# Performance work log

Hardware: AMD Instinct MI355X
Metric: run time of the kernel (lower is better)

## Reference

```python
import jax, jax.numpy as jnp
import numpy as np

D_MODEL = 1024
NUM_HEADS = 16
D_K = D_MODEL // NUM_HEADS


def setup_inputs() -> dict:
    key = jax.random.key(0)
    ks = jax.random.split(key, 7)
    B, S = 2, 2048
    query = jax.random.normal(ks[0], (B, S, D_MODEL), dtype=jnp.float32)
    key_t = jax.random.normal(ks[1], (B, S, D_MODEL), dtype=jnp.float32)
    value = jax.random.normal(ks[2], (B, S, D_MODEL), dtype=jnp.float32)
    attention_mask = jnp.ones((B, S), dtype=jnp.int32)
    # xavier_uniform for square d_model x d_model: limit = sqrt(6/(fan_in+fan_out))
    limit = np.sqrt(6.0 / (D_MODEL + D_MODEL)).astype(np.float32)
    def xav(k):
        return jax.random.uniform(k, (D_MODEL, D_MODEL), dtype=jnp.float32, minval=-limit, maxval=limit)
    return {
        "query": query, "key": key_t, "value": value,
        "attention_mask": attention_mask,
        "w_q": xav(ks[3]), "w_k": xav(ks[4]), "w_v": xav(ks[5]), "w_o": xav(ks[6]),
    }


def reference(query, key, value, attention_mask, w_q, w_k, w_v, w_o):
    B, S, _ = query.shape
    # torch Linear: x @ W.T  (weights stored [out, in])
    def proj(x, w):
        y = jnp.einsum('bsd,ed->bse', x, w)
        return y.reshape(B, S, NUM_HEADS, D_K).transpose(0, 2, 1, 3)  # [B,H,S,Dk]
    q = proj(query, w_q)
    k = proj(key, w_k)
    v = proj(value, w_v)
    scores = jnp.einsum('bhqd,bhkd->bhqk', q, k) / jnp.sqrt(jnp.float32(D_K))
    # mask [B,S] -> [B,1,1,S]; masked_fill where mask == 0
    mask = (attention_mask[:, None, None, :] == 0)
    scores = jnp.where(mask, jnp.float32(-1e9), scores)
    attn = jax.nn.softmax(scores, axis=-1)
    # dropout p=0.0 (eval) -> identity
    context = jnp.einsum('bhqk,bhkd->bhqd', attn, v)
    context = context.transpose(0, 2, 1, 3).reshape(B, S, D_MODEL)
    return jnp.einsum('bsd,ed->bse', context, w_o)
```

## Files before the change

### kernel.cpp

```cpp
#include <hip/hip_runtime.h>
#include <hip/hip_bf16.h>


typedef short short8  __attribute__((ext_vector_type(8)));
typedef short short4v __attribute__((ext_vector_type(4)));
typedef float f32x4   __attribute__((ext_vector_type(4)));

#define D_MODEL 1024
#define SEQ     2048
#define NHEAD   16
#define DKD     64
#define HSTR    (SEQ * DKD)
#define QSCALE  0.1803368801111204f
#define EXP2F(x) exp2f(x)

#define MFMA16(a, b, c) __builtin_amdgcn_mfma_f32_16x16x32_bf16((a), (b), (c), 0, 0, 0)

__device__ __forceinline__ ushort f2bf(float f) {
    __hip_bfloat16 h = __float2bfloat16(f);
    return __builtin_bit_cast(ushort, h);
}

__device__ __forceinline__ short8 frag128(const ushort* base, int row, int c0) {
    int cb = (c0 * 2) ^ ((row & 7) << 4);
    return *(const short8*)((const char*)base + row * 128 + cb);
}
__device__ __forceinline__ short8 frag256(const ushort* base, int row, int c0) {
    int cb = (c0 * 2) ^ ((row & 7) << 4);
    return *(const short8*)((const char*)base + row * 256 + cb);
}

__global__ __launch_bounds__(256) void cvt_w(
    const float* __restrict__ s0, const float* __restrict__ s1, const float* __restrict__ s2,
    ushort* __restrict__ dst)
{
    const int z = blockIdx.y;
    const float* s = (z == 0) ? s0 : ((z == 1) ? s1 : s2);
    ushort* d = dst + (size_t)z * 1048576;
    const int i = (blockIdx.x * 256 + threadIdx.x) * 8;
    f32x4 a = *(const f32x4*)(s + i);
    f32x4 b = *(const f32x4*)(s + i + 4);
    short8 o;
    #pragma unroll
    for (int u = 0; u < 4; ++u) { o[u] = (short)f2bf(a[u]); o[4 + u] = (short)f2bf(b[u]); }
    *(short8*)(d + i) = o;
}

template<int LAYOUT, int A_BF16>
__global__ __launch_bounds__(256, 3) void gemm_nt(
    const void* __restrict__ A0, const void* __restrict__ A1, const void* __restrict__ A2,
    const ushort* __restrict__ W0, const ushort* __restrict__ W1, const ushort* __restrict__ W2,
    void* __restrict__ O0, void* __restrict__ O1, void* __restrict__ O2)
{
    const int z = blockIdx.z;
    const void*   A = (z == 0) ? A0 : ((z == 1) ? A1 : A2);
    const ushort* W = (z == 0) ? W0 : ((z == 1) ? W1 : W2);
    void* O         = (z == 0) ? O0 : ((z == 1) ? O1 : O2);

    const int bm = blockIdx.x * 128;
    const int bn = blockIdx.y * 128;
    const int tid = threadIdx.x;
    const int w = tid >> 6, l = tid & 63;
    const int wr = w >> 1, wc = w & 1;

    __shared__ ushort sm[16384];

    f32x4 acc[4][4] = {};
    short8 areg[4], wreg[4];
    const int srow = tid >> 3;
    const int sc8  = (tid & 7) << 3;
    const int scb  = (sc8 * 2);

    #define GLOADT(t_) {                                                                    \
        _Pragma("unroll")                                                                   \
        for (int i = 0; i < 4; ++i) {                                                       \
            int row = i * 32 + srow;                                                        \
            if (A_BF16) {                                                                   \
                areg[i] = *(const short8*)((const ushort*)A + (size_t)(bm + row) * 1024 + (t_) * 64 + sc8); \
            } else {                                                                        \
                const float* ap = (const float*)A + (size_t)(bm + row) * 1024 + (t_) * 64 + sc8; \
                f32x4 x0 = *(const f32x4*)ap, x1 = *(const f32x4*)(ap + 4);                 \
                _Pragma("unroll")                                                           \
                for (int u = 0; u < 4; ++u) { areg[i][u] = (short)f2bf(x0[u]); areg[i][4 + u] = (short)f2bf(x1[u]); } \
            }                                                                               \
            wreg[i] = *(const short8*)(W + (size_t)(bn + row) * 1024 + (t_) * 64 + sc8);    \
        } }

    #define GWRITET() {                                                                     \
        _Pragma("unroll")                                                                   \
        for (int i = 0; i < 4; ++i) {                                                       \
            int row = i * 32 + srow;                                                        \
            int cb  = scb ^ ((row & 7) << 4);                                               \
            *(short8*)((char*)sm + row * 128 + cb) = areg[i];                               \
            *(short8*)((char*)(sm + 8192) + row * 128 + cb) = wreg[i];                      \
        } }

    GLOADT(0);
    #pragma unroll 1
    for (int t = 0; t < 16; ++t) {
        GWRITET();
        __syncthreads();
        if (t < 15) GLOADT(t + 1);

        #pragma unroll
        for (int kk = 0; kk < 2; ++kk) {
            const int c0 = kk * 32 + ((l >> 4) << 3);
            short8 af[4], bf[4];
            #pragma unroll
            for (int mi = 0; mi < 4; ++mi)
                af[mi] = frag128(sm, wr * 64 + mi * 16 + (l & 15), c0);
            #pragma unroll
            for (int ni = 0; ni < 4; ++ni)
                bf[ni] = frag128(sm + 8192, wc * 64 + ni * 16 + (l & 15), c0);
            #pragma unroll
            for (int mi = 0; mi < 4; ++mi)
                #pragma unroll
                for (int ni = 0; ni < 4; ++ni)
                    acc[mi][ni] = MFMA16(af[mi], bf[ni], acc[mi][ni]);
        }
        __syncthreads();
    }
    #undef GLOADT
    #undef GWRITET

    if (LAYOUT == 0 && z == 2) {
        #pragma unroll
        for (int mi = 0; mi < 4; ++mi) {
            #pragma unroll
            for (int ni = 0; ni < 4; ++ni) {
                int n_l = wc * 64 + ni * 16 + (l & 15);
                int m0  = wr * 64 + mi * 16 + ((l >> 4) << 2);
                short4v v4;
                #pragma unroll
                for (int j = 0; j < 4; ++j) v4[j] = (short)f2bf(acc[mi][ni][j]);
                *(short4v*)((char*)sm + n_l * 256 + ((m0 * 2) ^ ((n_l & 7) << 4))) = v4;
            }
        }
        __syncthreads();
        const int row = tid >> 1, half = tid & 1;
        const int n_g = bn + row;
        const int bb  = bm >> 11;
        ushort* Op = (ushort*)O + (size_t)(bb * NHEAD + (n_g >> 6)) * HSTR
                     + (size_t)(n_g & 63) * SEQ + (bm & 2047) + half * 64;
        #pragma unroll
        for (int u = 0; u < 8; ++u) {
            short8 c = *(const short8*)((char*)sm + row * 256
                        + (((half * 64 + u * 8) * 2) ^ ((row & 7) << 4)));
            *(short8*)(Op + u * 8) = c;
        }
        return;
    }

    const float sc = (LAYOUT == 0 && z == 0) ? QSCALE : 1.0f;
    #pragma unroll
    for (int mi = 0; mi < 4; ++mi) {
        #pragma unroll
        for (int ni = 0; ni < 4; ++ni) {
            #pragma unroll
            for (int j = 0; j < 4; ++j) {
                int m = bm + wr * 64 + mi * 16 + ((l >> 4) << 2) + j;
                int n = bn + wc * 64 + ni * 16 + (l & 15);
                if (LAYOUT == 0) {
                    int b = m >> 11, s = m & 2047, h = n >> 6, dk = n & 63;
                    ((ushort*)O)[(size_t)(b * NHEAD + h) * HSTR + s * DKD + dk] = f2bf(acc[mi][ni][j] * sc);
                } else {
                    ((float*)O)[(size_t)m * 1024 + n] = acc[mi][ni][j];
                }
            }
        }
    }
}

__global__ __launch_bounds__(256, 2) void attn_fwd(
    const ushort* __restrict__ Q, const ushort* __restrict__ K, const ushort* __restrict__ Vt,
    const int* __restrict__ mask, ushort* __restrict__ ctx)
{
    const int tid = threadIdx.x;
    const int w = tid >> 6, l = tid & 63;
    const int hi = l >> 4, lo = l & 15;
    const int id  = blockIdx.x;
    const int nid = (id & 7) * 64 + (id >> 3);
    const int bh  = nid >> 4;
    const int q0  = (nid & 15) * 128;
    const int b   = bh >> 4, h = bh & 15;

    __shared__ ushort sm[2][16384];
    __shared__ int mflag;

    if (tid == 0) mflag = 1;
    __syncthreads();
    {
        const int4* mp = ((const int4*)(mask + b * SEQ)) + tid;
        int4 m0 = mp[0], m1 = mp[256];
        if (!(m0.x && m0.y && m0.z && m0.w && m1.x && m1.y && m1.z && m1.w)) mflag = 0;
    }

    const ushort* Qh = Q  + (size_t)bh * HSTR;
    const ushort* Kh = K  + (size_t)bh * HSTR;
    const ushort* Vh = Vt + (size_t)bh * HSTR;

    short8 qf[2][2];
    #pragma unroll
    for (int g = 0; g < 2; ++g)
        #pragma unroll
        for (int kk = 0; kk < 2; ++kk)
            qf[g][kk] = *(const short8*)(Qh + (size_t)(q0 + w * 32 + g * 16 + lo) * DKD
                                         + kk * 32 + hi * 8);

    f32x4 acc[2][4] = {};
    float m_run[2] = {-INFINITY, -INFINITY}, l_run[2] = {0.0f, 0.0f};

    const int kr = tid >> 3;
    const int kc = (tid & 7) << 3;
    const int vr = tid >> 4;
    const int vkpb = (tid & 15) << 4;

    short8  kreg[4];
    short4v vreg0[4], vreg1[4];

    #define LOADT(kt_) {                                                                   \
        _Pragma("unroll")                                                                  \
        for (int i = 0; i < 4; ++i)                                                        \
            kreg[i] = *(const short8*)(Kh + (size_t)((kt_) * 128 + i * 32 + kr) * DKD + kc); \
        _Pragma("unroll")                                                                  \
        for (int i = 0; i < 4; ++i) {                                                      \
            const ushort* vp = Vh + (size_t)(i * 16 + vr) * SEQ + (kt_) * 128 + ((tid >> 2) & 3) * 32 + (tid & 3) * 4; \
            vreg0[i] = *(const short4v*)(vp);                                              \
            vreg1[i] = *(const short4v*)(vp + 16); } }

    #define WRITET(buf_) {                                                                 \
        _Pragma("unroll")                                                                  \
        for (int i = 0; i < 4; ++i) {                                                      \
            int r = i * 32 + kr;                                                           \
            *(short8*)((char*)sm[buf_] + r * 128 + ((kc * 2) ^ ((r & 7) << 4))) = kreg[i]; } \
        _Pragma("unroll")                                                                  \
        for (int i = 0; i < 4; ++i) {                                                      \
            int r = i * 16 + vr;                                                           \
            char* p = (char*)(sm[buf_] + 8192) + r * 256 + (vkpb ^ ((r & 7) << 4));        \
            *(short4v*)(p)     = vreg0[i];                                                 \
            *(short4v*)(p + 8) = vreg1[i]; } }

    LOADT(0); WRITET(0);
    __syncthreads();
    const bool allones = (mflag != 0);
    const f32x4 zf = {};

    #define SMG(g_) {                                                                      \
        if (!allones) {                                                                    \
            const int* mrow = mask + b * SEQ + kt * 128 + hi * 4;                          \
            _Pragma("unroll")                                                              \
            for (int ni = 0; ni < 8; ++ni) {                                               \
                int4 mv = *(const int4*)(mrow + ni * 16);                                  \
                s4[g_][ni][0] = mv.x ? s4[g_][ni][0] : -1e9f;                              \
                s4[g_][ni][1] = mv.y ? s4[g_][ni][1] : -1e9f;                              \
                s4[g_][ni][2] = mv.z ? s4[g_][ni][2] : -1e9f;                              \
                s4[g_][ni][3] = mv.w ? s4[g_][ni][3] : -1e9f;                              \
            }                                                                              \
        }                                                                                  \
        float t = fmaxf(fmaxf(s4[g_][0][0], s4[g_][0][1]), fmaxf(s4[g_][0][2], s4[g_][0][3])); \
        _Pragma("unroll")                                                                  \
        for (int ni = 1; ni < 8; ++ni) {                                                   \
            float tn = fmaxf(fmaxf(s4[g_][ni][0], s4[g_][ni][1]),                          \
                             fmaxf(s4[g_][ni][2], s4[g_][ni][3]));                         \
            t = fmaxf(t, tn);                                                              \
        }                                                                                  \
        t = fmaxf(t, __shfl_xor(t, 16));                                                   \
        t = fmaxf(t, __shfl_xor(t, 32));                                                   \
        if (!__all(t <= m_run[g_] + 8.0f)) {                                               \
            float mnew = fmaxf(m_run[g_], t);                                              \
            float c = EXP2F(m_run[g_] - mnew);                                             \
            m_run[g_] = mnew;                                                              \
            l_run[g_] *= c;                                                                \
            float cj[4];                                                                   \
            _Pragma("unroll")                                                              \
            for (int j = 0; j < 4; ++j) cj[j] = __shfl(c, (l & 48) | (hi * 4 + j));        \
            _Pragma("unroll")                                                              \
            for (int ni = 0; ni < 4; ++ni)                                                 \
                _Pragma("unroll")                                                          \
                for (int j = 0; j < 4; ++j) acc[g_][ni][j] *= cj[j];                       \
        }                                                                                  \
        float rs = 0.0f;                                                                   \
        _Pragma("unroll")                                                                  \
        for (int ni = 0; ni < 8; ++ni) {                                                   \
            _Pragma("unroll")                                                              \
            for (int j = 0; j < 4; ++j) s4[g_][ni][j] = EXP2F(s4[g_][ni][j] - m_run[g_]);  \
            rs += (s4[g_][ni][0] + s4[g_][ni][1]) + (s4[g_][ni][2] + s4[g_][ni][3]);       \
        }                                                                                  \
        rs += __shfl_xor(rs, 16);                                                          \
        rs += __shfl_xor(rs, 32);                                                          \
        l_run[g_] += rs;                                                                   \
        _Pragma("unroll")                                                                  \
        for (int kk = 0; kk < 4; ++kk)                                                     \
            _Pragma("unroll")                                                              \
            for (int j = 0; j < 4; ++j) {                                                  \
                pa[g_][kk][j]     = (short)f2bf(s4[g_][2 * kk][j]);                        \
                pa[g_][kk][4 + j] = (short)f2bf(s4[g_][2 * kk + 1][j]);                    \
            } }

    #pragma unroll 1
    for (int kt = 0; kt < 16; ++kt) {
        const int cur = kt & 1;
        const ushort* kb = sm[cur];
        const ushort* vb = sm[cur] + 8192;

        if (kt < 15) LOADT(kt + 1);

        f32x4 s4[2][8];
        __builtin_amdgcn_s_setprio(1);
        #pragma unroll
        for (int ni = 0; ni < 8; ++ni) {
            short8 kf = frag128(kb, ni * 16 + lo, hi * 8);
            s4[0][ni] = MFMA16(kf, qf[0][0], zf);
            s4[1][ni] = MFMA16(kf, qf[1][0], zf);
        }
        #pragma unroll
        for (int ni = 0; ni < 8; ++ni) {
            short8 kf = frag128(kb, ni * 16 + lo, 32 + hi * 8);
            s4[0][ni] = MFMA16(kf, qf[0][1], s4[0][ni]);
            s4[1][ni] = MFMA16(kf, qf[1][1], s4[1][ni]);
        }
        __builtin_amdgcn_s_setprio(0);

        short8 pa[2][4];
        SMG(0)
        SMG(1)

        if (kt < 15) WRITET(cur ^ 1);

        __builtin_amdgcn_s_setprio(1);
        #pragma unroll
        for (int kk = 0; kk < 4; ++kk) {
            const int c0 = kk * 32 + hi * 8;
            #pragma unroll
            for (int ni = 0; ni < 4; ++ni) {
                short8 vf = frag256(vb, ni * 16 + lo, c0);
                acc[0][ni] = MFMA16(pa[0][kk], vf, acc[0][ni]);
                acc[1][ni] = MFMA16(pa[1][kk], vf, acc[1][ni]);
            }
        }
        __builtin_amdgcn_s_setprio(0);

        __syncthreads();
    }
    #undef SMG
    #undef LOADT
    #undef WRITET

    #pragma unroll
    for (int g = 0; g < 2; ++g) {
        float inv = 1.0f / l_run[g];
        float invj[4];
        #pragma unroll
        for (int j = 0; j < 4; ++j)
            invj[j] = __shfl(inv, (l & 48) | (hi * 4 + j));
        #pragma unroll
        for (int ni = 0; ni < 4; ++ni)
            #pragma unroll
            for (int j = 0; j < 4; ++j) {
                int qg = q0 + w * 32 + g * 16 + hi * 4 + j;
                ctx[(size_t)(b * SEQ + qg) * D_MODEL + h * DKD + ni * 16 + lo] =
                    f2bf(acc[g][ni][j] * invj[j]);
            }
    }
}

__global__ void ws_sentinel(float* __restrict__ out, int n, float code) {
    int i = blockIdx.x * blockDim.x + threadIdx.x;
    if (i < n) out[i] = (i == 0) ? code : 0.0f;
}

extern "C" void kernel_launch(void* const* d_in, const int* in_sizes, int n_in,
                              void* d_out, int out_size, void* d_ws, size_t ws_size,
                              hipStream_t stream) {
    const float* q    = (const float*)d_in[0];
    const float* k    = (const float*)d_in[1];
    const float* v    = (const float*)d_in[2];
    const int*   mask = (const int*)d_in[3];
    const float* wq   = (const float*)d_in[4];
    const float* wk   = (const float*)d_in[5];
    const float* wv   = (const float*)d_in[6];
    const float* wo   = (const float*)d_in[7];
    float* out = (float*)d_out;

    if (ws_size < (size_t)33554432) {
        float code = 100.0f + (float)(ws_size >> 20);
        ws_sentinel<<<(out_size + 255) / 256, 256, 0, stream>>>(out, out_size, code);
        return;
    }

    ushort* ws = (ushort*)d_ws;
    ushort* Qb = ws;
    ushort* Kb = ws + 4194304;
    ushort* Vb = ws + 8388608;
    ushort* Cb = ws + 12582912;

    dim3 blk(256, 1, 1);
    cvt_w<<<dim3(512, 3), blk, 0, stream>>>(wq, wk, wv, Cb);
    gemm_nt<0, 0><<<dim3(32, 8, 3), blk, 0, stream>>>(
        q, k, v, Cb, Cb + 1048576, Cb + 2097152, Qb, Kb, Vb);
    attn_fwd<<<dim3(512, 1, 1), blk, 0, stream>>>(Qb, Kb, Vb, mask, Cb);
    cvt_w<<<dim3(512, 1), blk, 0, stream>>>(wo, wo, wo, Qb);
    gemm_nt<1, 1><<<dim3(32, 8, 1), blk, 0, stream>>>(
        Cb, Cb, Cb, Qb, Qb, Qb, out, out, out);
}
```

Baseline: 136.4 us.

## Split attention KV tile across two wave groups with LDS merge of partial softmax

Doubles the attention block to 512 threads: two groups of four waves each process half of every 128-key tile for the same query rows, keeping separate running max/sum and accumulators. The groups are merged at the end through shared memory using log-sum-exp rescaling. This halves per-wave register and instruction work per tile to raise occupancy and latency hiding, at the cost of a final LDS reduction and more waves contending for the same tiles. It also switches exp2 to the hardware builtin.

```diff
diff --git a/kernel.cpp b/kernel.cpp
--- a/kernel.cpp
+++ b/kernel.cpp
@@ -12,7 +12,7 @@
 #define DKD     64
 #define HSTR    (SEQ * DKD)
 #define QSCALE  0.1803368801111204f
-#define EXP2F(x) exp2f(x)
+#define EXP2F(x) __builtin_amdgcn_exp2f(x)
 
 #define MFMA16(a, b, c) __builtin_amdgcn_mfma_f32_16x16x32_bf16((a), (b), (c), 0, 0, 0)
 
@@ -171,13 +171,14 @@
     }
 }
 
-__global__ __launch_bounds__(256, 2) void attn_fwd(
+__global__ __launch_bounds__(512, 4) void attn_fwd(
     const ushort* __restrict__ Q, const ushort* __restrict__ K, const ushort* __restrict__ Vt,
     const int* __restrict__ mask, ushort* __restrict__ ctx)
 {
     const int tid = threadIdx.x;
     const int w = tid >> 6, l = tid & 63;
     const int hi = l >> 4, lo = l & 15;
+    const int g = w >> 2, wq = w & 3;
     const int id  = blockIdx.x;
     const int nid = (id & 7) * 64 + (id >> 3);
     const int bh  = nid >> 4;
@@ -190,9 +191,8 @@
     if (tid == 0) mflag = 1;
     __syncthreads();
     {
-        const int4* mp = ((const int4*)(mask + b * SEQ)) + tid;
-        int4 m0 = mp[0], m1 = mp[256];
-        if (!(m0.x && m0.y && m0.z && m0.w && m1.x && m1.y && m1.z && m1.w)) mflag = 0;
+        int4 m0 = ((const int4*)(mask + b * SEQ))[tid];
+        if (!(m0.x && m0.y && m0.z && m0.w)) mflag = 0;
     }
 
     const ushort* Qh = Q  + (size_t)bh * HSTR;
@@ -201,13 +201,13 @@
 
     short8 qf[2][2];
     #pragma unroll
-    for (int g = 0; g < 2; ++g)
+    for (int gq = 0; gq < 2; ++gq)
         #pragma unroll
         for (int kk = 0; kk < 2; ++kk)
-            qf[g][kk] = *(const short8*)(Qh + (size_t)(q0 + w * 32 + g * 16 + lo) * DKD
-                                         + kk * 32 + hi * 8);
-
-    f32x4 acc[2][4] = {};
+            qf[gq][kk] = *(const short8*)(Qh + (size_t)(q0 + wq * 32 + gq * 16 + lo) * DKD
+                                          + kk * 32 + hi * 8);
+
+    f32x4 acc_o[2][4] = {};
     float m_run[2] = {-INFINITY, -INFINITY}, l_run[2] = {0.0f, 0.0f};
 
     const int kr = tid >> 3;
@@ -215,27 +215,27 @@
     const int vr = tid >> 4;
     const int vkpb = (tid & 15) << 4;
 
-    short8  kreg[4];
-    short4v vreg0[4], vreg1[4];
+    short8  kreg[2];
+    short4v vreg0[2], vreg1[2];
 
     #define LOADT(kt_) {                                                                   \
         _Pragma("unroll")                                                                  \
-        for (int i = 0; i < 4; ++i)                                                        \
-            kreg[i] = *(const short8*)(Kh + (size_t)((kt_) * 128 + i * 32 + kr) * DKD + kc); \
-        _Pragma("unroll")                                                                  \
-        for (int i = 0; i < 4; ++i) {                                                      \
-            const ushort* vp = Vh + (size_t)(i * 16 + vr) * SEQ + (kt_) * 128 + ((tid >> 2) & 3) * 32 + (tid & 3) * 4; \
+        for (int i = 0; i < 2; ++i)                                                        \
+            kreg[i] = *(const short8*)(Kh + (size_t)((kt_) * 128 + i * 64 + kr) * DKD + kc); \
+        _Pragma("unroll")                                                                  \
+        for (int i = 0; i < 2; ++i) {                                                      \
+            const ushort* vp = Vh + (size_t)(i * 32 + vr) * SEQ + (kt_) * 128 + ((tid >> 2) & 3) * 32 + (tid & 3) * 4; \
             vreg0[i] = *(const short4v*)(vp);                                              \
             vreg1[i] = *(const short4v*)(vp + 16); } }
 
     #define WRITET(buf_) {                                                                 \
         _Pragma("unroll")                                                                  \
-        for (int i = 0; i < 4; ++i) {                                                      \
-            int r = i * 32 + kr;                                                           \
+        for (int i = 0; i < 2; ++i) {                                                      \
+            int r = i * 64 + kr;                                                           \
             *(short8*)((char*)sm[buf_] + r * 128 + ((kc * 2) ^ ((r & 7) << 4))) = kreg[i]; } \
         _Pragma("unroll")                                                                  \
-        for (int i = 0; i < 4; ++i) {                                                      \
-            int r = i * 16 + vr;                                                           \
+        for (int i = 0; i < 2; ++i) {                                                      \
+            int r = i * 32 + vr;                                                           \
             char* p = (char*)(sm[buf_] + 8192) + r * 256 + (vkpb ^ ((r & 7) << 4));        \
             *(short4v*)(p)     = vreg0[i];                                                 \
             *(short4v*)(p + 8) = vreg1[i]; } }
@@ -245,56 +245,44 @@
     const bool allones = (mflag != 0);
     const f32x4 zf = {};
 
-    #define SMG(g_) {                                                                      \
-        if (!allones) {                                                                    \
-            const int* mrow = mask + b * SEQ + kt * 128 + hi * 4;                          \
-            _Pragma("unroll")                                                              \
-            for (int ni = 0; ni < 8; ++ni) {                                               \
-                int4 mv = *(const int4*)(mrow + ni * 16);                                  \
-                s4[g_][ni][0] = mv.x ? s4[g_][ni][0] : -1e9f;                              \
-                s4[g_][ni][1] = mv.y ? s4[g_][ni][1] : -1e9f;                              \
-                s4[g_][ni][2] = mv.z ? s4[g_][ni][2] : -1e9f;                              \
-                s4[g_][ni][3] = mv.w ? s4[g_][ni][3] : -1e9f;                              \
-            }                                                                              \
-        }                                                                                  \
-        float t = fmaxf(fmaxf(s4[g_][0][0], s4[g_][0][1]), fmaxf(s4[g_][0][2], s4[g_][0][3])); \
-        _Pragma("unroll")                                                                  \
-        for (int ni = 1; ni < 8; ++ni) {                                                   \
-            float tn = fmaxf(fmaxf(s4[g_][ni][0], s4[g_][ni][1]),                          \
-                             fmaxf(s4[g_][ni][2], s4[g_][ni][3]));                         \
-            t = fmaxf(t, tn);                                                              \
-        }                                                                                  \
+    #define SMG(gq_) {                                                                     \
+        float t = fmaxf(fmaxf(s4[gq_][0][0], s4[gq_][0][1]),                               \
+                        fmaxf(s4[gq_][0][2], s4[gq_][0][3]));                              \
+        _Pragma("unroll")                                                                  \
+        for (int ni = 1; ni < 4; ++ni)                                                     \
+            t = fmaxf(t, fmaxf(fmaxf(s4[gq_][ni][0], s4[gq_][ni][1]),                      \
+                               fmaxf(s4[gq_][ni][2], s4[gq_][ni][3])));                    \
         t = fmaxf(t, __shfl_xor(t, 16));                                                   \
         t = fmaxf(t, __shfl_xor(t, 32));                                                   \
-        if (!__all(t <= m_run[g_] + 8.0f)) {                                               \
-            float mnew = fmaxf(m_run[g_], t);                                              \
-            float c = EXP2F(m_run[g_] - mnew);                                             \
-            m_run[g_] = mnew;                                                              \
-            l_run[g_] *= c;                                                                \
+        if (!__all(t <= m_run[gq_] + 8.0f)) {                                              \
+            float mnew = fmaxf(m_run[gq_], t);                                             \
+            float c = EXP2F(m_run[gq_] - mnew);                                            \
+            m_run[gq_] = mnew;                                                             \
+            l_run[gq_] *= c;                                                               \
             float cj[4];                                                                   \
             _Pragma("unroll")                                                              \
             for (int j = 0; j < 4; ++j) cj[j] = __shfl(c, (l & 48) | (hi * 4 + j));        \
             _Pragma("unroll")                                                              \
             for (int ni = 0; ni < 4; ++ni)                                                 \
                 _Pragma("unroll")                                                          \
-                for (int j = 0; j < 4; ++j) acc[g_][ni][j] *= cj[j];                       \
+                for (int j = 0; j < 4; ++j) acc_o[gq_][ni][j] *= cj[j];                    \
         }                                                                                  \
         float rs = 0.0f;                                                                   \
         _Pragma("unroll")                                                                  \
-        for (int ni = 0; ni < 8; ++ni) {                                                   \
+        for (int ni = 0; ni < 4; ++ni) {                                                   \
             _Pragma("unroll")                                                              \
-            for (int j = 0; j < 4; ++j) s4[g_][ni][j] = EXP2F(s4[g_][ni][j] - m_run[g_]);  \
-            rs += (s4[g_][ni][0] + s4[g_][ni][1]) + (s4[g_][ni][2] + s4[g_][ni][3]);       \
+            for (int j = 0; j < 4; ++j) s4[gq_][ni][j] = EXP2F(s4[gq_][ni][j] - m_run[gq_]); \
+            rs += (s4[gq_][ni][0] + s4[gq_][ni][1]) + (s4[gq_][ni][2] + s4[gq_][ni][3]);   \
         }                                                                                  \
         rs += __shfl_xor(rs, 16);                                                          \
         rs += __shfl_xor(rs, 32);                                                          \
-        l_run[g_] += rs;                                                                   \
-        _Pragma("unroll")                                                                  \
-        for (int kk = 0; kk < 4; ++kk)                                                     \
+        l_run[gq_] += rs;                                                                  \
+        _Pragma("unroll")                                                                  \
+        for (int kk = 0; kk < 2; ++kk)                                                     \
             _Pragma("unroll")                                                              \
             for (int j = 0; j < 4; ++j) {                                                  \
-                pa[g_][kk][j]     = (short)f2bf(s4[g_][2 * kk][j]);                        \
-                pa[g_][kk][4 + j] = (short)f2bf(s4[g_][2 * kk + 1][j]);                    \
+                pa[gq_][kk][j]     = (short)f2bf(s4[gq_][2 * kk][j]);                      \
+                pa[gq_][kk][4 + j] = (short)f2bf(s4[gq_][2 * kk + 1][j]);                  \
             } }
 
     #pragma unroll 1
@@ -305,23 +293,38 @@
 
         if (kt < 15) LOADT(kt + 1);
 
-        f32x4 s4[2][8];
+        f32x4 s4[2][4];
         __builtin_amdgcn_s_setprio(1);
         #pragma unroll
-        for (int ni = 0; ni < 8; ++ni) {
-            short8 kf = frag128(kb, ni * 16 + lo, hi * 8);
+        for (int ni = 0; ni < 4; ++ni) {
+            short8 kf = frag128(kb, g * 64 + ni * 16 + lo, hi * 8);
             s4[0][ni] = MFMA16(kf, qf[0][0], zf);
             s4[1][ni] = MFMA16(kf, qf[1][0], zf);
         }
         #pragma unroll
-        for (int ni = 0; ni < 8; ++ni) {
-            short8 kf = frag128(kb, ni * 16 + lo, 32 + hi * 8);
+        for (int ni = 0; ni < 4; ++ni) {
+            short8 kf = frag128(kb, g * 64 + ni * 16 + lo, 32 + hi * 8);
             s4[0][ni] = MFMA16(kf, qf[0][1], s4[0][ni]);
             s4[1][ni] = MFMA16(kf, qf[1][1], s4[1][ni]);
         }
         __builtin_amdgcn_s_setprio(0);
 
-        short8 pa[2][4];
+        if (!allones) {
+            const int* mrow = mask + b * SEQ + kt * 128 + g * 64 + hi * 4;
+            #pragma unroll
+            for (int ni = 0; ni < 4; ++ni) {
+                int4 mv = *(const int4*)(mrow + ni * 16);
+                #pragma unroll
+                for (int gq = 0; gq < 2; ++gq) {
+                    s4[gq][ni][0] = mv.x ? s4[gq][ni][0] : -1e9f;
+                    s4[gq][ni][1] = mv.y ? s4[gq][ni][1] : -1e9f;
+                    s4[gq][ni][2] = mv.z ? s4[gq][ni][2] : -1e9f;
+                    s4[gq][ni][3] = mv.w ? s4[gq][ni][3] : -1e9f;
+                }
+            }
+        }
+
+        short8 pa[2][2];
         SMG(0)
         SMG(1)
 
@@ -329,13 +332,13 @@
 
         __builtin_amdgcn_s_setprio(1);
         #pragma unroll
-        for (int kk = 0; kk < 4; ++kk) {
-            const int c0 = kk * 32 + hi * 8;
+        for (int kk = 0; kk < 2; ++kk) {
+            const int c0 = (g * 2 + kk) * 32 + hi * 8;
             #pragma unroll
             for (int ni = 0; ni < 4; ++ni) {
                 short8 vf = frag256(vb, ni * 16 + lo, c0);
-                acc[0][ni] = MFMA16(pa[0][kk], vf, acc[0][ni]);
-                acc[1][ni] = MFMA16(pa[1][kk], vf, acc[1][ni]);
+                acc_o[0][ni] = MFMA16(pa[0][kk], vf, acc_o[0][ni]);
+                acc_o[1][ni] = MFMA16(pa[1][kk], vf, acc_o[1][ni]);
             }
         }
         __builtin_amdgcn_s_setprio(0);
@@ -346,21 +349,44 @@
     #undef LOADT
     #undef WRITET
 
-    #pragma unroll
-    for (int g = 0; g < 2; ++g) {
-        float inv = 1.0f / l_run[g];
-        float invj[4];
-        #pragma unroll
-        for (int j = 0; j < 4; ++j)
-            invj[j] = __shfl(inv, (l & 48) | (hi * 4 + j));
-        #pragma unroll
-        for (int ni = 0; ni < 4; ++ni)
+    __syncthreads();
+    float* accs = (float*)sm;
+    float* mls  = (float*)sm + 4 * 64 * 33;
+    if (g == 1) {
+        float* ap = accs + (wq * 64 + l) * 33;
+        #pragma unroll
+        for (int gq = 0; gq < 2; ++gq)
+            #pragma unroll
+            for (int ni = 0; ni < 4; ++ni)
+                #pragma unroll
+                for (int j = 0; j < 4; ++j)
+                    ap[gq * 16 + ni * 4 + j] = acc_o[gq][ni][j];
+        float* mp = mls + (wq * 64 + l) * 4;
+        mp[0] = m_run[0]; mp[1] = m_run[1]; mp[2] = l_run[0]; mp[3] = l_run[1];
+    }
+    __syncthreads();
+    if (g == 0) {
+        const float* ap = accs + (wq * 64 + l) * 33;
+        const float* mp = mls + (wq * 64 + l) * 4;
+        #pragma unroll
+        for (int gq = 0; gq < 2; ++gq) {
+            float mB = mp[gq], lB = mp[2 + gq];
+            float ms = fmaxf(m_run[gq], mB);
+            float cA = EXP2F(m_run[gq] - ms), cB = EXP2F(mB - ms);
+            float inv = 1.0f / (cA * l_run[gq] + cB * lB);
+            float sA = cA * inv, sB = cB * inv;
             #pragma unroll
             for (int j = 0; j < 4; ++j) {
-                int qg = q0 + w * 32 + g * 16 + hi * 4 + j;
-                ctx[(size_t)(b * SEQ + qg) * D_MODEL + h * DKD + ni * 16 + lo] =
-                    f2bf(acc[g][ni][j] * invj[j]);
+                float sAr = __shfl(sA, (l & 48) | (hi * 4 + j));
+                float sBr = __shfl(sB, (l & 48) | (hi * 4 + j));
+                int qg = q0 + wq * 32 + gq * 16 + hi * 4 + j;
+                #pragma unroll
+                for (int ni = 0; ni < 4; ++ni) {
+                    float v = sAr * acc_o[gq][ni][j] + sBr * ap[gq * 16 + ni * 4 + j];
+                    ctx[(size_t)(b * SEQ + qg) * D_MODEL + h * DKD + ni * 16 + lo] = f2bf(v);
+                }
             }
+        }
     }
 }
 
@@ -398,7 +424,7 @@
     cvt_w<<<dim3(512, 3), blk, 0, stream>>>(wq, wk, wv, Cb);
     gemm_nt<0, 0><<<dim3(32, 8, 3), blk, 0, stream>>>(
         q, k, v, Cb, Cb + 1048576, Cb + 2097152, Qb, Kb, Vb);
-    attn_fwd<<<dim3(512, 1, 1), blk, 0, stream>>>(Qb, Kb, Vb, mask, Cb);
+    attn_fwd<<<dim3(512, 1, 1), dim3(512, 1, 1), 0, stream>>>(Qb, Kb, Vb, mask, Cb);
     cvt_w<<<dim3(512, 1), blk, 0, stream>>>(wo, wo, wo, Qb);
     gemm_nt<1, 1><<<dim3(32, 8, 1), blk, 0, stream>>>(
         Cb, Cb, Cb, Qb, Qb, Qb, out, out, out);
```

New measurement: 132.3 us. 3.0% less time.
